# Optimization experiments

Measured on AMD Instinct MI355X. Metric: run time of the kernel, lower is better.

## Reference

```python
import jax, jax.numpy as jnp
import numpy as np

N_NODES = 100000
N_EDGES = 3200000
IN_CH = 256
OUT_CH = 64
HEADS = 2
NEG_SLOPE = 0.2  # PyG GATConv default


def setup_inputs() -> dict:
    key = jax.random.key(0)
    k1, k2, k3, k4, k5 = jax.random.split(key, 5)
    z = jax.random.normal(k1, (N_NODES, IN_CH), dtype=jnp.float32)
    edge_index = jax.random.randint(k2, (2, N_EDGES), 0, N_NODES, dtype=jnp.int64)
    # Glorot-ish scaled params
    W = jax.random.normal(k3, (IN_CH, HEADS * OUT_CH), dtype=jnp.float32) / np.sqrt(IN_CH)
    att_src = jax.random.normal(k4, (1, HEADS, OUT_CH), dtype=jnp.float32) / np.sqrt(OUT_CH)
    att_dst = jax.random.normal(k5, (1, HEADS, OUT_CH), dtype=jnp.float32) / np.sqrt(OUT_CH)
    bias = jnp.zeros((OUT_CH,), dtype=jnp.float32)
    return {"z": z, "edge_index": edge_index, "W": W,
            "att_src": att_src, "att_dst": att_dst, "bias": bias}


def reference(z, edge_index, W, att_src, att_dst, bias):
    # PyG GATConv forward (eval mode: attention dropout is identity),
    # add_self_loops=True, concat=False (mean over heads), no activation.
    n = z.shape[0]
    loop = jnp.arange(n, dtype=edge_index.dtype)
    src = jnp.concatenate([edge_index[0], loop])  # (Etot,)
    dst = jnp.concatenate([edge_index[1], loop])

    x = (z @ W).reshape(n, HEADS, OUT_CH)  # per-head projected features (n,H,C)
    a_src = jnp.sum(x * att_src, axis=-1)  # (n,H)
    a_dst = jnp.sum(x * att_dst, axis=-1)  # (n,H)

    logits = a_src[src] + a_dst[dst]       # (Etot,H)
    logits = jax.nn.leaky_relu(logits, NEG_SLOPE)

    # segment softmax over edges grouped by destination node
    seg_max = jax.ops.segment_max(logits, dst, num_segments=n)   # (n,H)
    e = jnp.exp(logits - seg_max[dst])
    seg_sum = jax.ops.segment_sum(e, dst, num_segments=n)        # (n,H)
    alpha = e / seg_sum[dst]                                     # (Etot,H)

    msgs = x[src] * alpha[:, :, None]                            # (Etot,H,C)
    out = jax.ops.segment_sum(msgs, dst, num_segments=n)         # (n,H,C)
    out = out.mean(axis=1) + bias                                # concat=False -> mean
    return out
```

## Files before the change

kernel.cpp:

```cpp
#include <hip/hip_runtime.h>
#include <hip/hip_bf16.h>
#include <hip/hip_fp16.h>

#define IN_CH   256
#define NOUT    128
#define OUT_CH  64
#define NEG     0.2f

#define XQMAX   5.5f
#define QS      (127.0f / XQMAX)
#define SINV    (XQMAX / 127.0f)

#define NBINS     256
#define BIN_SHIFT 9
#define NPB       512
#define CAPB      18432
#define EPT       16
#define GSTRIDE   32

typedef __attribute__((ext_vector_type(8))) short bf16x8;
typedef __attribute__((ext_vector_type(4))) float f32x4;

static __device__ __forceinline__ short f2bf(float f) {
    __hip_bfloat16 h = __float2bfloat16(f);
    return *reinterpret_cast<short*>(&h);
}

static __device__ __forceinline__ int pack_e(float l0, float l1) {
    __half2 h2;
    h2.x = __float2half(__expf(l0));
    h2.y = __float2half(__expf(l1));
    return *reinterpret_cast<int*>(&h2);
}

static __device__ __forceinline__ signed char q8(float v) {
    float q = rintf(v * QS);
    q = fminf(127.f, fmaxf(-127.f, q));
    return (signed char)(int)q;
}

__global__ void k_transpose_w(const float* __restrict__ W,
                              __hip_bfloat16* __restrict__ Wt,
                              int* __restrict__ gcnt) {
    int i = blockIdx.x * blockDim.x + threadIdx.x;
    if (blockIdx.x < 32) gcnt[blockIdx.x * 256 + threadIdx.x] = 0;
    if (blockIdx.x == 32 && threadIdx.x == 0) gcnt[NBINS * GSTRIDE] = 0;
    if (i < IN_CH * NOUT) {
        int n = i >> 8, k = i & 255;
        Wt[i] = __float2bfloat16(W[k * NOUT + n]);
    }
}

__global__ __launch_bounds__(256) void k_gemm_pass1(
        const float* __restrict__ z,
        const __hip_bfloat16* __restrict__ wt,
        const float* __restrict__ att_s,
        const float* __restrict__ att_d,
        signed char* __restrict__ xq,
        float* __restrict__ a_src, float* __restrict__ a_dst,
        int nTiles, int gemmBlocks,
        const int* __restrict__ ei,
        int* __restrict__ gcnt, int* __restrict__ binned, int E) {
    __shared__ int lhist[NBINS];
    __shared__ int lscan[NBINS];
    __shared__ int lbase[NBINS];
    __shared__ int lplace[NBINS];
    __shared__ int lptr[NBINS];
    __shared__ int sEnt[256 * EPT];
    __shared__ unsigned char sBin[256 * EPT];

    if (blockIdx.x < (unsigned)gemmBlocks) {
        int wid  = (blockIdx.x * blockDim.x + threadIdx.x) >> 6;
        if (wid >= nTiles) return;
        int lane = threadIdx.x & 63;
        int m = lane & 15, quad = lane >> 4;
        int rbase = wid * 16;
        const float* zp = z + (size_t)(rbase + m) * IN_CH + quad * 8;
        const short* wp = (const short*)wt + m * IN_CH + quad * 8;
        f32x4 acc[8] = {};
#pragma unroll
        for (int kb = 0; kb < 8; ++kb) {
            float4 f0 = *(const float4*)(zp + kb * 32);
            float4 f1 = *(const float4*)(zp + kb * 32 + 4);
            bf16x8 a;
            a[0] = f2bf(f0.x); a[1] = f2bf(f0.y); a[2] = f2bf(f0.z); a[3] = f2bf(f0.w);
            a[4] = f2bf(f1.x); a[5] = f2bf(f1.y); a[6] = f2bf(f1.z); a[7] = f2bf(f1.w);
#pragma unroll
            for (int n = 0; n < 8; ++n) {
                bf16x8 b = *(const bf16x8*)(wp + n * 16 * IN_CH + kb * 32);
                acc[n] = __builtin_amdgcn_mfma_f32_16x16x32_bf16(a, b, acc[n], 0, 0, 0);
            }
        }
#pragma unroll
        for (int n = 0; n < 8; ++n)
#pragma unroll
            for (int r = 0; r < 4; ++r) {
                int row = rbase + quad * 4 + r;
                xq[(size_t)row * NOUT + n * 16 + m] = q8(acc[n][r]);
            }
        float asv[8], adv[8];
#pragma unroll
        for (int n = 0; n < 8; ++n) {
            asv[n] = att_s[n * 16 + m];
            adv[n] = att_d[n * 16 + m];
        }
        float ps0[4] = {}, ps1[4] = {}, pd0[4] = {}, pd1[4] = {};
#pragma unroll
        for (int r = 0; r < 4; ++r)
#pragma unroll
            for (int n = 0; n < 4; ++n) {
                ps0[r] += acc[n][r] * asv[n];
                ps1[r] += acc[n + 4][r] * asv[n + 4];
                pd0[r] += acc[n][r] * adv[n];
                pd1[r] += acc[n + 4][r] * adv[n + 4];
            }
#pragma unroll
        for (int msk = 1; msk < 16; msk <<= 1)
#pragma unroll
            for (int r = 0; r < 4; ++r) {
                ps0[r] += __shfl_xor(ps0[r], msk);
                ps1[r] += __shfl_xor(ps1[r], msk);
                pd0[r] += __shfl_xor(pd0[r], msk);
                pd1[r] += __shfl_xor(pd1[r], msk);
            }
        if (m < 4) {
            int r = m;
            int row = rbase + quad * 4 + r;
            ((float2*)a_src)[row] = make_float2(ps0[r], ps1[r]);
            ((float2*)a_dst)[row] = make_float2(pd0[r], pd1[r]);
        }
    } else {
        int t = threadIdx.x;
        int base = (blockIdx.x - gemmBlocks) * (256 * EPT);
        int nvalid = E - base;
        if (nvalid > 256 * EPT) nvalid = 256 * EPT;
        if (nvalid < 0) nvalid = 0;
        lhist[t] = 0;
        __syncthreads();

        int ent[EPT], bn[EPT];
#pragma unroll
        for (int j = 0; j < EPT; ++j) {
            int e = base + j * 256 + t;
            bn[j] = -1;
            if (e < E) {
                int s = ei[e], d = ei[E + e];
                ent[j] = ((d & (NPB - 1)) << 17) | s;
                bn[j]  = d >> BIN_SHIFT;
                atomicAdd(&lhist[bn[j]], 1);
            }
        }
        __syncthreads();
        lscan[t] = lhist[t];
        __syncthreads();
        for (int off = 1; off < NBINS; off <<= 1) {
            int u = (t >= off) ? lscan[t - off] : 0;
            __syncthreads();
            lscan[t] += u;
            __syncthreads();
        }
        {
            int c  = lhist[t];
            int b0 = lscan[t] - c;
            lbase[t]  = b0;
            lplace[t] = b0;
            lptr[t]   = (c > 0) ? atomicAdd(&gcnt[t * GSTRIDE], c) : 0;
        }
        __syncthreads();
#pragma unroll
        for (int j = 0; j < EPT; ++j) {
            if (bn[j] >= 0) {
                int pos = atomicAdd(&lplace[bn[j]], 1);
                sEnt[pos] = ent[j];
                sBin[pos] = (unsigned char)bn[j];
            }
        }
        __syncthreads();
        for (int i = t; i < nvalid; i += 256) {
            int b = sBin[i];
            int gpos = lptr[b] + (i - lbase[b]);
            if (gpos < CAPB)
                binned[(size_t)b * CAPB + gpos] = sEnt[i];
        }
    }
}

__global__ __launch_bounds__(1024) void k_pass2(
        const int* __restrict__ binned, const int* __restrict__ gcnt,
        int* __restrict__ gtot,
        const float* __restrict__ a_src, const float* __restrict__ a_dst,
        int2* __restrict__ epk, int* __restrict__ offsB, int* __restrict__ offsE, int N) {
    __shared__ int    lh[NPB];
    __shared__ int    lx[NPB];
    __shared__ float2 sad[NPB];
    __shared__ int    sBase;
    int b = blockIdx.x, t = threadIdx.x;
    int nodes = N - b * NPB;
    nodes = (nodes < 0) ? 0 : ((nodes > NPB) ? NPB : nodes);
    if (nodes == 0) return;
    int cnt = gcnt[b * GSTRIDE];
    if (cnt > CAPB) cnt = CAPB;
    const int* src = binned + (size_t)b * CAPB;

    if (t == 0) sBase = atomicAdd(gtot, cnt + nodes);
    if (t < NPB) {
        lh[t] = (t < nodes) ? 1 : 0;
        if (t < nodes) sad[t] = ((const float2*)a_dst)[b * NPB + t];
    }
    __syncthreads();
    for (int i = t; i < cnt; i += 1024)
        atomicAdd(&lh[(src[i] >> 17) & (NPB - 1)], 1);
    __syncthreads();
    if (t < NPB) lx[t] = lh[t];
    __syncthreads();
    for (int off = 1; off < NPB; off <<= 1) {
        int u = (t < NPB && t >= off) ? lx[t - off] : 0;
        __syncthreads();
        if (t < NPB) lx[t] += u;
        __syncthreads();
    }
    int base = sBase;
    int excl = 0;
    if (t < NPB) excl = lx[t] - lh[t];
    __syncthreads();
    if (t < NPB) lh[t] = excl + 1;
    __syncthreads();
    if (t < nodes) {
        int d = b * NPB + t;
        float2 as = ((const float2*)a_src)[d];
        float2 ad = sad[t];
        float l0 = as.x + ad.x; l0 = (l0 > 0.f) ? l0 : NEG * l0;
        float l1 = as.y + ad.y; l1 = (l1 > 0.f) ? l1 : NEG * l1;
        epk[base + excl] = make_int2(pack_e(l0, l1), d);
        offsB[d] = base + excl;
        offsE[d] = base + lx[t];
    }
    for (int i = t; i < cnt; i += 1024) {
        int ent = src[i];
        int dLow = (ent >> 17) & (NPB - 1);
        int s = ent & 0x1FFFF;
        float2 as = ((const float2*)a_src)[s];
        float2 ad = sad[dLow];
        float l0 = as.x + ad.x; l0 = (l0 > 0.f) ? l0 : NEG * l0;
        float l1 = as.y + ad.y; l1 = (l1 > 0.f) ? l1 : NEG * l1;
        int pos = atomicAdd(&lh[dLow], 1);
        epk[base + pos] = make_int2(pack_e(l0, l1), s);
    }
}

__global__ __launch_bounds__(256) void k_gat_agg(
        const int2* __restrict__ epk,
        const int* __restrict__ offsB, const int* __restrict__ offsE,
        const signed char* __restrict__ xq, const float* __restrict__ bias,
        float* __restrict__ out, int N) {
    int wid  = (blockIdx.x * blockDim.x + threadIdx.x) >> 6;
    if (wid >= N) return;
    int lane = threadIdx.x & 63;
    int beg = offsB[wid], end = offsE[wid];
    int half = lane >> 5;
    int sl   = lane & 31;
    unsigned hs = (unsigned)((sl >> 4) << 4);
    const unsigned* xv = (const unsigned*)xq;

    float ax[8] = {}, dn[2] = {};
    int i = beg;
    for (; i + 7 < end; i += 8) {
        int2 p[4];
#pragma unroll
        for (int u = 0; u < 4; ++u) p[u] = epk[i + 2 * u + half];
        float e[4]; unsigned F[4];
#pragma unroll
        for (int u = 0; u < 4; ++u) {
            e[u] = __half2float(__ushort_as_half(
                       (unsigned short)((unsigned)p[u].x >> hs)));
            F[u] = xv[(size_t)p[u].y * 32 + sl];
        }
#pragma unroll
        for (int u = 0; u < 4; ++u) {
            int c = (u & 1) * 4;
            ax[c + 0] += e[u] * (float)(signed char)(F[u]);
            ax[c + 1] += e[u] * (float)(signed char)(F[u] >> 8);
            ax[c + 2] += e[u] * (float)(signed char)(F[u] >> 16);
            ax[c + 3] += e[u] * (float)((int)F[u] >> 24);
            dn[u & 1] += e[u];
        }
    }
    for (; i + 1 < end; i += 2) {
        int2 p = epk[i + half];
        float e = __half2float(__ushort_as_half(
                      (unsigned short)((unsigned)p.x >> hs)));
        unsigned F = xv[(size_t)p.y * 32 + sl];
        ax[0] += e * (float)(signed char)(F);
        ax[1] += e * (float)(signed char)(F >> 8);
        ax[2] += e * (float)(signed char)(F >> 16);
        ax[3] += e * (float)((int)F >> 24);
        dn[0] += e;
    }
    if (i < end) {
        int2 p = epk[end - 1];
        float e = __half2float(__ushort_as_half(
                      (unsigned short)((unsigned)p.x >> hs)));
        e = half ? 0.f : e;
        unsigned F = xv[(size_t)p.y * 32 + sl];
        ax[0] += e * (float)(signed char)(F);
        ax[1] += e * (float)(signed char)(F >> 8);
        ax[2] += e * (float)(signed char)(F >> 16);
        ax[3] += e * (float)((int)F >> 24);
        dn[0] += e;
    }

    float a0 = ax[0] + ax[4], a1 = ax[1] + ax[5];
    float a2 = ax[2] + ax[6], a3 = ax[3] + ax[7];
    float d  = dn[0] + dn[1];
    a0 += __shfl_xor(a0, 32); a1 += __shfl_xor(a1, 32);
    a2 += __shfl_xor(a2, 32); a3 += __shfl_xor(a3, 32);
    d  += __shfl_xor(d, 32);
    float inv = 1.f / d;
    a0 *= inv; a1 *= inv; a2 *= inv; a3 *= inv;
    float b0 = __shfl_xor(a0, 16), b1 = __shfl_xor(a1, 16);
    float b2 = __shfl_xor(a2, 16), b3 = __shfl_xor(a3, 16);
    if (lane < 16) {
        int c = 4 * lane;
        const float hsc = 0.5f * SINV;
        float4 o;
        o.x = hsc * (a0 + b0) + bias[c + 0];
        o.y = hsc * (a1 + b1) + bias[c + 1];
        o.z = hsc * (a2 + b2) + bias[c + 2];
        o.w = hsc * (a3 + b3) + bias[c + 3];
        ((float4*)out)[(size_t)wid * 16 + lane] = o;
    }
}

extern "C" void kernel_launch(void* const* d_in, const int* in_sizes, int n_in,
                              void* d_out, int out_size, void* d_ws, size_t ws_size,
                              hipStream_t stream) {
    const float* z     = (const float*)d_in[0];
    const int*   ei    = (const int*)d_in[1];
    const float* W     = (const float*)d_in[2];
    const float* att_s = (const float*)d_in[3];
    const float* att_d = (const float*)d_in[4];
    const float* bias  = (const float*)d_in[5];
    float* out = (float*)d_out;

    const int N = in_sizes[0] / IN_CH;
    const int E = in_sizes[1] / 2;
    const int Etot = E + N;

    size_t off = 0;
    auto alloc = [&](size_t bytes) {
        void* p = (char*)d_ws + off;
        off += (bytes + 255) & ~(size_t)255;
        return p;
    };
    signed char* xq      = (signed char*)alloc((size_t)N * NOUT);
    __hip_bfloat16* Wt   = (__hip_bfloat16*)alloc((size_t)IN_CH * NOUT * 2);
    float* a_src         = (float*)alloc((size_t)N * 2 * 4);
    float* a_dst         = (float*)alloc((size_t)N * 2 * 4);
    int*   gcnt          = (int*)alloc((NBINS * GSTRIDE + 256) * 4);
    int*   gtot          = gcnt + NBINS * GSTRIDE;
    int*   offsB         = (int*)alloc((size_t)N * 4);
    int*   offsE         = (int*)alloc((size_t)N * 4);
    int*   binned        = (int*)alloc((size_t)NBINS * CAPB * 4);
    int2*  epk           = (int2*)alloc((size_t)Etot * 8);
    (void)ws_size;

    const int nTiles = N / 16;
    const int gemmBlocks = (nTiles + 3) / 4;
    const int p1Blocks = (E + 256 * EPT - 1) / (256 * EPT);

    k_transpose_w<<<(IN_CH * NOUT + 255) / 256, 256, 0, stream>>>(W, Wt, gcnt);
    k_gemm_pass1<<<gemmBlocks + p1Blocks, 256, 0, stream>>>(
        z, Wt, att_s, att_d, xq, a_src, a_dst, nTiles, gemmBlocks,
        ei, gcnt, binned, E);
    k_pass2<<<NBINS, 1024, 0, stream>>>(binned, gcnt, gtot, a_src, a_dst, epk, offsB, offsE, N);
    k_gat_agg<<<(N + 3) / 4, 256, 0, stream>>>(epk, offsB, offsE, xq, bias, out, N);
}
```

Before: 365.9 us.

## Split GEMM and edge binning into separate kernels with lighter binning pass

The fused GEMM/edge-binning kernel is split into two launches, so the GEMM blocks no longer carry the binning pass's large shared-memory footprint. The binning kernel halves edges per thread, replaces the barrier-heavy shared scan with a wave shuffle scan, and precomputes global scatter indices instead of storing per-entry bin bytes. These aim to raise occupancy and cut synchronisation. The cost is an extra kernel launch, the loss of overlap between GEMM and binning, and twice as many binning blocks hitting the global atomics.

```diff
diff --git a/kernel.cpp b/kernel.cpp
--- a/kernel.cpp
+++ b/kernel.cpp
@@ -15,7 +15,7 @@
 #define BIN_SHIFT 9
 #define NPB       512
 #define CAPB      18432
-#define EPT       16
+#define EPT       8
 #define GSTRIDE   32
 
 typedef __attribute__((ext_vector_type(8))) short bf16x8;
@@ -51,137 +51,135 @@
     }
 }
 
-__global__ __launch_bounds__(256) void k_gemm_pass1(
+__global__ __launch_bounds__(256) void k_gemm_x(
         const float* __restrict__ z,
         const __hip_bfloat16* __restrict__ wt,
         const float* __restrict__ att_s,
         const float* __restrict__ att_d,
         signed char* __restrict__ xq,
-        float* __restrict__ a_src, float* __restrict__ a_dst,
-        int nTiles, int gemmBlocks,
+        float* __restrict__ a_src, float* __restrict__ a_dst, int nTiles) {
+    int wid  = (blockIdx.x * blockDim.x + threadIdx.x) >> 6;
+    if (wid >= nTiles) return;
+    int lane = threadIdx.x & 63;
+    int m = lane & 15, quad = lane >> 4;
+    int rbase = wid * 16;
+    const float* zp = z + (size_t)(rbase + m) * IN_CH + quad * 8;
+    const short* wp = (const short*)wt + m * IN_CH + quad * 8;
+    f32x4 acc[8] = {};
+#pragma unroll
+    for (int kb = 0; kb < 8; ++kb) {
+        float4 f0 = *(const float4*)(zp + kb * 32);
+        float4 f1 = *(const float4*)(zp + kb * 32 + 4);
+        bf16x8 a;
+        a[0] = f2bf(f0.x); a[1] = f2bf(f0.y); a[2] = f2bf(f0.z); a[3] = f2bf(f0.w);
+        a[4] = f2bf(f1.x); a[5] = f2bf(f1.y); a[6] = f2bf(f1.z); a[7] = f2bf(f1.w);
+#pragma unroll
+        for (int n = 0; n < 8; ++n) {
+            bf16x8 b = *(const bf16x8*)(wp + n * 16 * IN_CH + kb * 32);
+            acc[n] = __builtin_amdgcn_mfma_f32_16x16x32_bf16(a, b, acc[n], 0, 0, 0);
+        }
+    }
+#pragma unroll
+    for (int n = 0; n < 8; ++n)
+#pragma unroll
+        for (int r = 0; r < 4; ++r) {
+            int row = rbase + quad * 4 + r;
+            xq[(size_t)row * NOUT + n * 16 + m] = q8(acc[n][r]);
+        }
+    float asv[8], adv[8];
+#pragma unroll
+    for (int n = 0; n < 8; ++n) {
+        asv[n] = att_s[n * 16 + m];
+        adv[n] = att_d[n * 16 + m];
+    }
+    float ps0[4] = {}, ps1[4] = {}, pd0[4] = {}, pd1[4] = {};
+#pragma unroll
+    for (int r = 0; r < 4; ++r)
+#pragma unroll
+        for (int n = 0; n < 4; ++n) {
+            ps0[r] += acc[n][r] * asv[n];
+            ps1[r] += acc[n + 4][r] * asv[n + 4];
+            pd0[r] += acc[n][r] * adv[n];
+            pd1[r] += acc[n + 4][r] * adv[n + 4];
+        }
+#pragma unroll
+    for (int msk = 1; msk < 16; msk <<= 1)
+#pragma unroll
+        for (int r = 0; r < 4; ++r) {
+            ps0[r] += __shfl_xor(ps0[r], msk);
+            ps1[r] += __shfl_xor(ps1[r], msk);
+            pd0[r] += __shfl_xor(pd0[r], msk);
+            pd1[r] += __shfl_xor(pd1[r], msk);
+        }
+    if (m < 4) {
+        int r = m;
+        int row = rbase + quad * 4 + r;
+        ((float2*)a_src)[row] = make_float2(ps0[r], ps1[r]);
+        ((float2*)a_dst)[row] = make_float2(pd0[r], pd1[r]);
+    }
+}
+
+__global__ __launch_bounds__(256) void k_pass1(
         const int* __restrict__ ei,
         int* __restrict__ gcnt, int* __restrict__ binned, int E) {
     __shared__ int lhist[NBINS];
-    __shared__ int lscan[NBINS];
-    __shared__ int lbase[NBINS];
     __shared__ int lplace[NBINS];
-    __shared__ int lptr[NBINS];
+    __shared__ int lresv[NBINS];
+    __shared__ int wsum[4];
     __shared__ int sEnt[256 * EPT];
-    __shared__ unsigned char sBin[256 * EPT];
-
-    if (blockIdx.x < (unsigned)gemmBlocks) {
-        int wid  = (blockIdx.x * blockDim.x + threadIdx.x) >> 6;
-        if (wid >= nTiles) return;
-        int lane = threadIdx.x & 63;
-        int m = lane & 15, quad = lane >> 4;
-        int rbase = wid * 16;
-        const float* zp = z + (size_t)(rbase + m) * IN_CH + quad * 8;
-        const short* wp = (const short*)wt + m * IN_CH + quad * 8;
-        f32x4 acc[8] = {};
-#pragma unroll
-        for (int kb = 0; kb < 8; ++kb) {
-            float4 f0 = *(const float4*)(zp + kb * 32);
-            float4 f1 = *(const float4*)(zp + kb * 32 + 4);
-            bf16x8 a;
-            a[0] = f2bf(f0.x); a[1] = f2bf(f0.y); a[2] = f2bf(f0.z); a[3] = f2bf(f0.w);
-            a[4] = f2bf(f1.x); a[5] = f2bf(f1.y); a[6] = f2bf(f1.z); a[7] = f2bf(f1.w);
-#pragma unroll
-            for (int n = 0; n < 8; ++n) {
-                bf16x8 b = *(const bf16x8*)(wp + n * 16 * IN_CH + kb * 32);
-                acc[n] = __builtin_amdgcn_mfma_f32_16x16x32_bf16(a, b, acc[n], 0, 0, 0);
-            }
-        }
-#pragma unroll
-        for (int n = 0; n < 8; ++n)
-#pragma unroll
-            for (int r = 0; r < 4; ++r) {
-                int row = rbase + quad * 4 + r;
-                xq[(size_t)row * NOUT + n * 16 + m] = q8(acc[n][r]);
-            }
-        float asv[8], adv[8];
-#pragma unroll
-        for (int n = 0; n < 8; ++n) {
-            asv[n] = att_s[n * 16 + m];
-            adv[n] = att_d[n * 16 + m];
-        }
-        float ps0[4] = {}, ps1[4] = {}, pd0[4] = {}, pd1[4] = {};
-#pragma unroll
-        for (int r = 0; r < 4; ++r)
-#pragma unroll
-            for (int n = 0; n < 4; ++n) {
-                ps0[r] += acc[n][r] * asv[n];
-                ps1[r] += acc[n + 4][r] * asv[n + 4];
-                pd0[r] += acc[n][r] * adv[n];
-                pd1[r] += acc[n + 4][r] * adv[n + 4];
-            }
-#pragma unroll
-        for (int msk = 1; msk < 16; msk <<= 1)
-#pragma unroll
-            for (int r = 0; r < 4; ++r) {
-                ps0[r] += __shfl_xor(ps0[r], msk);
-                ps1[r] += __shfl_xor(ps1[r], msk);
-                pd0[r] += __shfl_xor(pd0[r], msk);
-                pd1[r] += __shfl_xor(pd1[r], msk);
-            }
-        if (m < 4) {
-            int r = m;
-            int row = rbase + quad * 4 + r;
-            ((float2*)a_src)[row] = make_float2(ps0[r], ps1[r]);
-            ((float2*)a_dst)[row] = make_float2(pd0[r], pd1[r]);
-        }
-    } else {
-        int t = threadIdx.x;
-        int base = (blockIdx.x - gemmBlocks) * (256 * EPT);
-        int nvalid = E - base;
-        if (nvalid > 256 * EPT) nvalid = 256 * EPT;
-        if (nvalid < 0) nvalid = 0;
-        lhist[t] = 0;
-        __syncthreads();
-
-        int ent[EPT], bn[EPT];
-#pragma unroll
-        for (int j = 0; j < EPT; ++j) {
-            int e = base + j * 256 + t;
-            bn[j] = -1;
-            if (e < E) {
-                int s = ei[e], d = ei[E + e];
-                ent[j] = ((d & (NPB - 1)) << 17) | s;
-                bn[j]  = d >> BIN_SHIFT;
-                atomicAdd(&lhist[bn[j]], 1);
-            }
-        }
-        __syncthreads();
-        lscan[t] = lhist[t];
-        __syncthreads();
-        for (int off = 1; off < NBINS; off <<= 1) {
-            int u = (t >= off) ? lscan[t - off] : 0;
-            __syncthreads();
-            lscan[t] += u;
-            __syncthreads();
-        }
-        {
-            int c  = lhist[t];
-            int b0 = lscan[t] - c;
-            lbase[t]  = b0;
-            lplace[t] = b0;
-            lptr[t]   = (c > 0) ? atomicAdd(&gcnt[t * GSTRIDE], c) : 0;
-        }
-        __syncthreads();
-#pragma unroll
-        for (int j = 0; j < EPT; ++j) {
-            if (bn[j] >= 0) {
-                int pos = atomicAdd(&lplace[bn[j]], 1);
-                sEnt[pos] = ent[j];
-                sBin[pos] = (unsigned char)bn[j];
-            }
-        }
-        __syncthreads();
-        for (int i = t; i < nvalid; i += 256) {
-            int b = sBin[i];
-            int gpos = lptr[b] + (i - lbase[b]);
-            if (gpos < CAPB)
-                binned[(size_t)b * CAPB + gpos] = sEnt[i];
-        }
+    __shared__ int sIdx[256 * EPT];
+    int t = threadIdx.x;
+    int lane = t & 63, wv = t >> 6;
+    int base = blockIdx.x * (256 * EPT);
+    int nvalid = E - base;
+    if (nvalid > 256 * EPT) nvalid = 256 * EPT;
+    if (nvalid < 0) nvalid = 0;
+    lhist[t] = 0;
+    __syncthreads();
+
+    int ent[EPT], bn[EPT];
+#pragma unroll
+    for (int j = 0; j < EPT; ++j) {
+        int e = base + j * 256 + t;
+        bn[j] = -1;
+        if (e < E) {
+            int s = ei[e], d = ei[E + e];
+            ent[j] = ((d & (NPB - 1)) << 17) | s;
+            bn[j]  = d >> BIN_SHIFT;
+            atomicAdd(&lhist[bn[j]], 1);
+        }
+    }
+    __syncthreads();
+    int c = lhist[t];
+    int v = c;
+#pragma unroll
+    for (int d = 1; d < 64; d <<= 1) {
+        int u = __shfl_up(v, d);
+        if (lane >= d) v += u;
+    }
+    if (lane == 63) wsum[wv] = v;
+    __syncthreads();
+    int add = 0;
+#pragma unroll
+    for (int w = 0; w < 3; ++w) add += (wv > w) ? wsum[w] : 0;
+    int b0 = v + add - c;
+    lplace[t] = b0;
+    int gbase = (c > 0) ? atomicAdd(&gcnt[t * GSTRIDE], c) : 0;
+    lresv[t] = gbase - b0;
+    __syncthreads();
+#pragma unroll
+    for (int j = 0; j < EPT; ++j) {
+        if (bn[j] >= 0) {
+            int pos = atomicAdd(&lplace[bn[j]], 1);
+            sEnt[pos] = ent[j];
+            int gp = lresv[bn[j]] + pos;
+            sIdx[pos] = (gp < CAPB) ? (bn[j] * CAPB + gp) : -1;
+        }
+    }
+    __syncthreads();
+    for (int i = t; i < nvalid; i += 256) {
+        int gi = sIdx[i];
+        if (gi >= 0) binned[gi] = sEnt[i];
     }
 }
 
@@ -369,9 +367,8 @@
     const int p1Blocks = (E + 256 * EPT - 1) / (256 * EPT);
 
     k_transpose_w<<<(IN_CH * NOUT + 255) / 256, 256, 0, stream>>>(W, Wt, gcnt);
-    k_gemm_pass1<<<gemmBlocks + p1Blocks, 256, 0, stream>>>(
-        z, Wt, att_s, att_d, xq, a_src, a_dst, nTiles, gemmBlocks,
-        ei, gcnt, binned, E);
+    k_gemm_x<<<gemmBlocks, 256, 0, stream>>>(z, Wt, att_s, att_d, xq, a_src, a_dst, nTiles);
+    k_pass1<<<p1Blocks, 256, 0, stream>>>(ei, gcnt, binned, E);
     k_pass2<<<NBINS, 1024, 0, stream>>>(binned, gcnt, gtot, a_src, a_dst, epk, offsB, offsE, N);
     k_gat_agg<<<(N + 3) / 4, 256, 0, stream>>>(epk, offsB, offsE, xq, bias, out, N);
 }
```

Result: slower. 380.6 us (+4.0%).
